# Kernel optimization log

Hardware: AMD Instinct MI355X
Metric: run time of the kernel (lower is better)

## Reference

```python
import jax, jax.numpy as jnp
import numpy as np
import math

B, S, DIM = 4, 1024, 4096
N_HEADS, N_KV_HEADS = 32, 8
HEAD_DIM = DIM // N_HEADS  # 128
PAST = 1024
N_REP = N_HEADS // N_KV_HEADS


def _rope_freqs(seq_len, head_dim, theta=10000.0):
    inv = 1.0 / (theta ** (np.arange(0, head_dim, 2, dtype=np.float32) / head_dim))
    t = np.arange(seq_len, dtype=np.float32)
    ang = np.outer(t, inv)  # (S, head_dim//2)
    return jnp.asarray(np.cos(ang)), jnp.asarray(np.sin(ang))


def setup_inputs() -> dict:
    key = jax.random.key(0)
    ks = jax.random.split(key, 8)
    sc = 0.02
    x = jax.random.normal(ks[0], (B, S, DIM), dtype=jnp.float32)
    freqs_cos, freqs_sin = _rope_freqs(S, HEAD_DIM)
    cache_k = jax.random.normal(ks[1], (B, N_KV_HEADS, PAST, HEAD_DIM), dtype=jnp.float32)
    cache_v = jax.random.normal(ks[2], (B, N_KV_HEADS, PAST, HEAD_DIM), dtype=jnp.float32)
    wq = jax.random.normal(ks[3], (DIM, DIM), dtype=jnp.float32) * sc
    wk = jax.random.normal(ks[4], (N_KV_HEADS * HEAD_DIM, DIM), dtype=jnp.float32) * sc
    wv = jax.random.normal(ks[5], (N_KV_HEADS * HEAD_DIM, DIM), dtype=jnp.float32) * sc
    wo = jax.random.normal(ks[6], (DIM, DIM), dtype=jnp.float32) * sc
    return {"x": x, "freqs_cos": freqs_cos, "freqs_sin": freqs_sin,
            "cache_k": cache_k, "cache_v": cache_v,
            "wq": wq, "wk": wk, "wv": wv, "wo": wo}


def _apply_rotary(x, cos, sin):
    # x: (b, h, s, d); cos/sin: (s, d//2) broadcast to (1, 1, s, d//2)
    xr = x.reshape(*x.shape[:-1], -1, 2)
    x_r, x_i = xr[..., 0], xr[..., 1]
    cos = cos[None, None, :, :]
    sin = sin[None, None, :, :]
    out_r = x_r * cos - x_i * sin
    out_i = x_r * sin + x_i * cos
    return jnp.stack([out_r, out_i], axis=-1).reshape(x.shape)


def reference(x, freqs_cos, freqs_sin, cache_k, cache_v, wq, wk, wv, wo):
    bsz, seqlen, _ = x.shape
    xq = x @ wq.T  # (b, s, n_heads*hd)
    xk = x @ wk.T  # (b, s, n_kv*hd)
    xv = x @ wv.T
    xq = xq.reshape(bsz, seqlen, N_HEADS, HEAD_DIM).transpose(0, 2, 1, 3)
    xk = xk.reshape(bsz, seqlen, N_KV_HEADS, HEAD_DIM).transpose(0, 2, 1, 3)
    xv = xv.reshape(bsz, seqlen, N_KV_HEADS, HEAD_DIM).transpose(0, 2, 1, 3)
    xq = _apply_rotary(xq, freqs_cos, freqs_sin)
    xk = _apply_rotary(xk, freqs_cos, freqs_sin)
    keys = jnp.concatenate([cache_k, xk], axis=2)    # (b, kvh, past+s, hd)
    values = jnp.concatenate([cache_v, xv], axis=2)
    keys = jnp.repeat(keys, N_REP, axis=1)            # (b, h, kv, hd)
    values = jnp.repeat(values, N_REP, axis=1)
    scores = jnp.einsum('bhsd,bhkd->bhsk', xq, keys) / math.sqrt(HEAD_DIM)
    scores = jax.nn.softmax(scores, axis=-1)          # no mask (inference path)
    out = jnp.einsum('bhsk,bhkd->bhsd', scores, values)
    out = out.transpose(0, 2, 1, 3).reshape(bsz, seqlen, -1)
    return out @ wo.T
```

## Files before the change

### kernel.cpp

```cpp
#include <hip/hip_runtime.h>
#include <hip/hip_bf16.h>

using bf16 = __hip_bfloat16;
typedef __attribute__((ext_vector_type(4))) float f4;
typedef __attribute__((ext_vector_type(16))) float f16v;
typedef __attribute__((ext_vector_type(8))) short s8v;
typedef __attribute__((ext_vector_type(4))) short s4v;
typedef __attribute__((ext_vector_type(4))) unsigned int u4v;
typedef unsigned int u32;

__device__ __forceinline__ short f2bf(float x) {
  bf16 h = __float2bfloat16(x);
  return *reinterpret_cast<short*>(&h);
}

__device__ __forceinline__ u32 pkbf(float lo, float hi) {
  return (u32)(unsigned short)f2bf(lo) | ((u32)(unsigned short)f2bf(hi) << 16);
}

__device__ __forceinline__ void gload16(const bf16* g, bf16* l) {
  __builtin_amdgcn_global_load_lds(
      (const __attribute__((address_space(1))) u32*)g,
      (__attribute__((address_space(3))) u32*)l, 16, 0, 0);
}

__device__ __forceinline__ void swp32(u32& a, u32& b, int h) {
#if __has_builtin(__builtin_amdgcn_permlane32_swap)
  typedef __attribute__((ext_vector_type(2))) int i2v;
  i2v r = __builtin_amdgcn_permlane32_swap((int)a, (int)b, false, false);
  a = (u32)r.x;
  b = (u32)r.y;
#else
  u32 as = (u32)__shfl_xor((int)a, 32), bs = (u32)__shfl_xor((int)b, 32);
  u32 an = h ? bs : a, bn = h ? b : as;
  a = an;
  b = bn;
#endif
}

__device__ __forceinline__ float xhalf_max(float x) {
#if __has_builtin(__builtin_amdgcn_permlane32_swap)
  typedef __attribute__((ext_vector_type(2))) int i2v;
  i2v r = __builtin_amdgcn_permlane32_swap(__float_as_int(x), __float_as_int(x),
                                           false, false);
  return fmaxf(__int_as_float(r.x), __int_as_float(r.y));
#else
  return fmaxf(x, __shfl_xor(x, 32));
#endif
}
__device__ __forceinline__ float xhalf_sum(float x) {
#if __has_builtin(__builtin_amdgcn_permlane32_swap)
  typedef __attribute__((ext_vector_type(2))) int i2v;
  i2v r = __builtin_amdgcn_permlane32_swap(__float_as_int(x), __float_as_int(x),
                                           false, false);
  return __int_as_float(r.x) + __int_as_float(r.y);
#else
  return x + __shfl_xor(x, 32);
#endif
}

__global__ __launch_bounds__(256) void cvt_bf16(const float* __restrict__ src,
                                                bf16* __restrict__ dst) {
  size_t e = ((size_t)blockIdx.x * 256 + threadIdx.x) << 3;
  f4 a = *(const f4*)(src + e);
  f4 b = *(const f4*)(src + e + 4);
  s8v r = { f2bf(a[0]), f2bf(a[1]), f2bf(a[2]), f2bf(a[3]),
            f2bf(b[0]), f2bf(b[1]), f2bf(b[2]), f2bf(b[3]) };
  *(s8v*)(dst + e) = r;
}

__global__ __launch_bounds__(256) void cvt_cache_k(const float* __restrict__ src,
                                                   bf16* __restrict__ dst) {
  size_t e = ((size_t)blockIdx.x * 256 + threadIdx.x) << 2;
  f4 v = *(const f4*)(src + e);
  unsigned d = (unsigned)(e & 127u), p = (unsigned)((e >> 7) & 1023u), bk = (unsigned)(e >> 17);
  s4v r = { f2bf(v[0]), f2bf(v[1]), f2bf(v[2]), f2bf(v[3]) };
  *(s4v*)(dst + (((size_t)bk * 2048 + p) << 7) + d) = r;
}

__global__ __launch_bounds__(256) void cvt_cache_v(const float* __restrict__ src,
                                                   bf16* __restrict__ dst) {
  size_t e = ((size_t)blockIdx.x * 256 + threadIdx.x) << 2;
  unsigned p = (unsigned)(e & 1023u), d = (unsigned)((e >> 10) & 127u), bk = (unsigned)(e >> 17);
  const float* s = src + (((size_t)bk * 1024 + p) << 7) + d;
  s4v r = { f2bf(s[0]), f2bf(s[128]), f2bf(s[256]), f2bf(s[384]) };
  *(s4v*)(dst + (((size_t)bk * 128 + d) << 11) + p) = r;
}

__global__ __launch_bounds__(256) void rope_kernel(bf16* __restrict__ buf,
                                                   const float* __restrict__ fc,
                                                   const float* __restrict__ fs,
                                                   int sstride, int soff) {
  size_t t = (size_t)blockIdx.x * 256 + threadIdx.x;
  unsigned ip = (unsigned)(t & 63u);
  unsigned s  = (unsigned)((t >> 6) & 1023u);
  unsigned hh = (unsigned)(t >> 16);
  size_t base = ((size_t)hh * sstride + soff + s) * 128 + 2 * ip;
  unsigned u = *(unsigned*)(buf + base);
  float xr = __uint_as_float(u << 16);
  float xi = __uint_as_float(u & 0xffff0000u);
  float c = fc[s * 64 + ip], sn = fs[s * 64 + ip];
  unsigned short r0 = (unsigned short)f2bf(xr * c - xi * sn);
  unsigned short r1 = (unsigned short)f2bf(xr * sn + xi * c);
  *(unsigned*)(buf + base) = (unsigned)r0 | ((unsigned)r1 << 16);
}

#define MODE_QKV 0
#define MODE_OUT 1

#define PHASE_TAIL(AC, BC, KS, MH)                                           \
  {                                                                          \
    s8v af[4], bv[4];                                                        \
    const int cofs = ((((KS) * 4) | g) ^ fx) << 3;                           \
    _Pragma("unroll") for (int mi = 0; mi < 4; ++mi)                         \
        af[mi] = *(const s8v*)&(AC)[aRowBase + ((MH)*4 + mi) * 1024 + cofs]; \
    _Pragma("unroll") for (int ni = 0; ni < 4; ++ni)                         \
        bv[ni] = *(const s8v*)&(BC)[bRowBase + ni * 1024 + cofs];            \
    __builtin_amdgcn_s_barrier();                                            \
    asm volatile("s_waitcnt lgkmcnt(0)" ::: "memory");                       \
    __builtin_amdgcn_s_setprio(1);                                           \
    _Pragma("unroll") for (int mi = 0; mi < 4; ++mi)                         \
      _Pragma("unroll") for (int ni = 0; ni < 4; ++ni)                       \
          acc[(MH)*4 + mi][ni] = __builtin_amdgcn_mfma_f32_16x16x32_bf16(    \
              af[mi], bv[ni], acc[(MH)*4 + mi][ni], 0, 0, 0);                \
    __builtin_amdgcn_s_setprio(0);                                           \
    __builtin_amdgcn_s_barrier();                                            \
  }

#define PHASE_HEAD(AC, BC)                                                   \
  {                                                                          \
    __builtin_amdgcn_s_barrier();                                            \
    s8v af[4], bv[4];                                                        \
    const int cofs = (g ^ fx) << 3;                                          \
    _Pragma("unroll") for (int mi = 0; mi < 4; ++mi)                         \
        af[mi] = *(const s8v*)&(AC)[aRowBase + mi * 1024 + cofs];            \
    _Pragma("unroll") for (int ni = 0; ni < 4; ++ni)                         \
        bv[ni] = *(const s8v*)&(BC)[bRowBase + ni * 1024 + cofs];            \
    asm volatile("s_waitcnt lgkmcnt(0)" ::: "memory");                       \
    __builtin_amdgcn_s_setprio(1);                                           \
    _Pragma("unroll") for (int mi = 0; mi < 4; ++mi)                         \
      _Pragma("unroll") for (int ni = 0; ni < 4; ++ni)                       \
          acc[mi][ni] = __builtin_amdgcn_mfma_f32_16x16x32_bf16(             \
              af[mi], bv[ni], acc[mi][ni], 0, 0, 0);                         \
    __builtin_amdgcn_s_setprio(0);                                           \
    __builtin_amdgcn_s_barrier();                                            \
  }

#define KTILE(AC, BC, PA, PB, NA, NB, PF)                                    \
  {                                                                          \
    if (PF) { gload16((NA), (PA)); gload16((NA) + rstep, (PA) + 4096); }     \
    if (PF) asm volatile("s_waitcnt vmcnt(2)" ::: "memory");                 \
    else    asm volatile("s_waitcnt vmcnt(0)" ::: "memory");                 \
    PHASE_HEAD(AC, BC)                                                       \
    if (PF) { gload16((NA) + 2 * rstep, (PA) + 8192);                        \
              gload16((NA) + 3 * rstep, (PA) + 12288); }                     \
    PHASE_TAIL(AC, BC, 0, 1)                                                 \
    if (PF) { gload16((NB), (PB)); gload16((NB) + rstep, (PB) + 4096); }     \
    PHASE_TAIL(AC, BC, 1, 0)                                                 \
    if (PF) { gload16((NB) + 2 * rstep, (PB) + 8192);                        \
              gload16((NB) + 3 * rstep, (PB) + 12288); }                     \
    PHASE_TAIL(AC, BC, 1, 1)                                                 \
  }

template <int MODE>
__global__ __launch_bounds__(512, 2) void gemm256(const bf16* __restrict__ A,
                                                  const bf16* __restrict__ B,
                                                  void* __restrict__ o1,
                                                  void* __restrict__ o2,
                                                  void* __restrict__ o3,
                                                  int K, float scale) {
  extern __shared__ bf16 smem[];
  bf16* A0 = smem;
  bf16* A1 = smem + 16384;
  bf16* B0 = smem + 32768;
  bf16* B1 = smem + 49152;

  const int tid = threadIdx.x;
  const int lane = tid & 63;
  const int wid = tid >> 6;
  const int wm = wid >> 2, wn = wid & 3;
  const int fr = lane & 15;
  const int g = lane >> 4;
  const int rg = g << 2;
  const int fx = lane & 7;

  const int gy = gridDim.y;
  int lin = blockIdx.y * gridDim.x + blockIdx.x;
  const int qq = (gridDim.x * gy) >> 3;
  lin = (lin & 7) * qq + (lin >> 3);
  const int bm = lin / gy;
  const int bn = lin % gy;

  const int r0 = tid >> 3;
  const int sc = (tid & 7) ^ (r0 & 7);
  const bf16* aptr = A + (size_t)(bm * 256 + r0) * K + sc * 8;
  const bf16* bptr = B + (size_t)(bn * 256 + r0) * K + sc * 8;
  const size_t rstep = (size_t)64 * K;
  const int wofs = (tid & 448) << 3;
  bf16* pA0 = A0 + wofs; bf16* pA1 = A1 + wofs;
  bf16* pB0 = B0 + wofs; bf16* pB1 = B1 + wofs;

  const int aRowBase = (wm * 128 + fr) * 64;
  const int bRowBase = (wn * 64 + fr) * 64;

  f4 acc[8][4] = {};

#pragma unroll
  for (int i = 0; i < 4; ++i) gload16(aptr + i * rstep, pA0 + i * 4096);
#pragma unroll
  for (int i = 0; i < 4; ++i) gload16(bptr + i * rstep, pB0 + i * 4096);

  const int nk = K >> 6;
  for (int kt = 0; kt < nk; kt += 2) {
    const bf16* na = aptr + (kt + 1) * 64;
    const bf16* nb = bptr + (kt + 1) * 64;
    KTILE(A0, B0, pA1, pB1, na, nb, true)
    const bool pf2 = (kt + 2 < nk);
    const bf16* na2 = aptr + (kt + 2) * 64;
    const bf16* nb2 = bptr + (kt + 2) * 64;
    KTILE(A1, B1, pA0, pB0, na2, nb2, pf2)
  }

#pragma unroll
  for (int m = 0; m < 8; ++m) {
    const int grow0 = bm * 256 + wm * 128 + m * 16 + rg;
    const int b = grow0 >> 10, s0 = grow0 & 1023;
#pragma unroll
    for (int n = 0; n < 4; ++n) {
      const int gcol = bn * 256 + wn * 64 + n * 16 + fr;
      if constexpr (MODE == MODE_OUT) {
#pragma unroll
        for (int j = 0; j < 4; ++j)
          ((float*)o1)[(size_t)(grow0 + j) * 4096 + gcol] = acc[m][n][j];
      } else {
        if (gcol < 4096) {
          const int h = gcol >> 7, d = gcol & 127;
#pragma unroll
          for (int j = 0; j < 4; ++j)
            ((bf16*)o1)[((((size_t)b * 32 + h) << 10) + s0 + j) * 128 + d] =
                __float2bfloat16(acc[m][n][j] * scale);
        } else if (gcol < 5120) {
          const int c = gcol - 4096, hv = c >> 7, d = c & 127;
#pragma unroll
          for (int j = 0; j < 4; ++j)
            ((bf16*)o2)[(((size_t)b * 8 + hv) * 2048 + 1024 + s0 + j) * 128 + d] =
                __float2bfloat16(acc[m][n][j]);
        } else {
          const int c = gcol - 5120, hv = c >> 7, d = c & 127;
          s4v r = { f2bf(acc[m][n][0]), f2bf(acc[m][n][1]),
                    f2bf(acc[m][n][2]), f2bf(acc[m][n][3]) };
          *(s4v*)((bf16*)o3 + (((size_t)b * 8 + hv) * 128 + d) * 2048 + 1024 + s0) = r;
        }
      }
    }
  }
}

__global__ __launch_bounds__(512) void attn_kernel(const bf16* __restrict__ Q,
                                                   const bf16* __restrict__ Kf,
                                                   const bf16* __restrict__ Vt,
                                                   bf16* __restrict__ O) {
  __shared__ alignas(16) bf16 Kls[2][8192];
  __shared__ alignas(16) bf16 Vls[2][8192];

  const int tid = threadIdx.x;
  const int lane = tid & 63;
  const int w = tid >> 6;
  const int h = lane >> 5;
  const int q31 = lane & 31;
  const int rx = q31 & 7;

  const int qb = blockIdx.x;
  const int bh = blockIdx.y;
  const int b = bh >> 5, hd = bh & 31;
  const int kv = hd >> 2;

  const size_t qbase = (((size_t)b * 32 + hd) << 10) * 128;
  const size_t kbase = (((size_t)b * 8 + kv) * 2048) * 128;
  const size_t vbase = (((size_t)b * 8 + kv) * 128) * 2048;

  const int qrow = qb * 256 + w * 32 + q31;
  s8v qf[8];
#pragma unroll
  for (int c = 0; c < 8; ++c)
    qf[c] = *(const s8v*)&Q[qbase + (size_t)qrow * 128 + c * 16 + h * 8];

  const int sr = tid >> 3;
  const int swz8 = (((tid & 7) ^ (sr & 7)) << 3);
  const int wbase = w * 512;

  f16v oacc[4] = {};
  float mrun = -3e38f, lrun = 0.f;

  auto stage = [&](int kb, int bufi) {
    const bf16* ksrc = Kf + kbase + (size_t)(kb * 64 + sr) * 128 + swz8;
    gload16(ksrc,      &Kls[bufi][wbase]);
    gload16(ksrc + 64, &Kls[bufi][4096 + wbase]);
    const bf16* vsrc = Vt + vbase + (size_t)sr * 2048 + kb * 64 + swz8;
    gload16(vsrc,                      &Vls[bufi][wbase]);
    gload16(vsrc + (size_t)64 * 2048,  &Vls[bufi][4096 + wbase]);
  };

  stage(0, 0);
  asm volatile("s_waitcnt vmcnt(0)" ::: "memory");
  __syncthreads();

  for (int kb = 0; kb < 32; ++kb) {
    const int bufi = kb & 1;
    if (kb + 1 < 32) stage(kb + 1, bufi ^ 1);

    const bf16* KB = Kls[bufi];
    const bf16* VB = Vls[bufi];

    f16v sac[2] = {};
    __builtin_amdgcn_s_setprio(1);
#pragma unroll
    for (int c = 0; c < 8; ++c) {
      const int cc = 2 * c + h;
      const int cof = (cc >> 3) * 4096 + (((cc & 7) ^ rx) << 3);
      s8v k0 = *(const s8v*)&KB[cof + q31 * 64];
      s8v k1 = *(const s8v*)&KB[cof + (32 + q31) * 64];
      sac[0] = __builtin_amdgcn_mfma_f32_32x32x16_bf16(k0, qf[c], sac[0], 0, 0, 0);
      sac[1] = __builtin_amdgcn_mfma_f32_32x32x16_bf16(k1, qf[c], sac[1], 0, 0, 0);
    }
    __builtin_amdgcn_s_setprio(0);

    float pm = -3e38f;
#pragma unroll
    for (int r = 0; r < 16; ++r) {
      pm = fmaxf(pm, sac[0][r]);
      pm = fmaxf(pm, sac[1][r]);
    }
    pm = xhalf_max(pm);

    const bool skip = __all(pm <= mrun + 8.0f);
    if (!skip) {
      const float mnew = fmaxf(mrun, pm);
      const float corr = exp2f(mrun - mnew);
      mrun = mnew;
      lrun *= corr;
#pragma unroll
      for (int m = 0; m < 4; ++m)
#pragma unroll
        for (int r = 0; r < 16; ++r) oacc[m][r] *= corr;
    }
    float ls = 0.f;
#pragma unroll
    for (int s = 0; s < 2; ++s)
#pragma unroll
      for (int r = 0; r < 16; ++r) {
        const float p = exp2f(sac[s][r] - mrun);
        sac[s][r] = p;
        ls += p;
      }
    lrun += xhalf_sum(ls);

    s8v F[4];
#pragma unroll
    for (int s = 0; s < 2; ++s) {
      u32 W[8];
#pragma unroll
      for (int t = 0; t < 8; ++t) W[t] = pkbf(sac[s][2 * t], sac[s][2 * t + 1]);
      swp32(W[0], W[2], h); swp32(W[1], W[3], h);
      swp32(W[4], W[6], h); swp32(W[5], W[7], h);
      union { u32 u[4]; s8v v; } f0, f1;
      f0.u[0] = W[0]; f0.u[1] = W[1]; f0.u[2] = W[2]; f0.u[3] = W[3];
      f1.u[0] = W[4]; f1.u[1] = W[5]; f1.u[2] = W[6]; f1.u[3] = W[7];
      F[s * 2] = f0.v;
      F[s * 2 + 1] = f1.v;
    }

    __builtin_amdgcn_s_setprio(1);
#pragma unroll
    for (int ksg = 0; ksg < 4; ++ksg) {
      const int cc2 = 2 * ksg + h;
      const int vof = ((cc2 ^ rx) << 3);
#pragma unroll
      for (int m = 0; m < 4; ++m) {
        s8v vf = *(const s8v*)&VB[(m * 32 + q31) * 64 + vof];
        oacc[m] = __builtin_amdgcn_mfma_f32_32x32x16_bf16(vf, F[ksg], oacc[m], 0, 0, 0);
      }
    }
    __builtin_amdgcn_s_setprio(0);

    asm volatile("s_waitcnt vmcnt(0)" ::: "memory");
    __syncthreads();
  }

  const float inv = 1.f / lrun;
  bf16* orow = O + ((size_t)b * 1024 + qrow) * 4096 + hd * 128;
#pragma unroll
  for (int m = 0; m < 4; ++m)
#pragma unroll
    for (int r = 0; r < 16; r += 2) {
      const int d = m * 32 + (r & 3) + 8 * (r >> 2) + 4 * h;
      *(u32*)&orow[d] = pkbf(oacc[m][r] * inv, oacc[m][r + 1] * inv);
    }
}

extern "C" void kernel_launch(void* const* d_in, const int* in_sizes, int n_in,
                              void* d_out, int out_size, void* d_ws, size_t ws_size,
                              hipStream_t stream) {
  const float* x  = (const float*)d_in[0];
  const float* fc = (const float*)d_in[1];
  const float* fs = (const float*)d_in[2];
  const float* ck = (const float*)d_in[3];
  const float* cv = (const float*)d_in[4];
  const float* wq = (const float*)d_in[5];
  const float* wk = (const float*)d_in[6];
  const float* wv = (const float*)d_in[7];
  const float* wo = (const float*)d_in[8];
  float* out = (float*)d_out;

  char* ws = (char*)d_ws;
  bf16* qr    = (bf16*)(ws);
  bf16* kfull = (bf16*)(ws + (32u << 20));
  bf16* vt    = (bf16*)(ws + (48u << 20));
  bf16* xb    = (bf16*)(ws + (64u << 20));
  bf16* attn  = xb;
  bf16* wqb   = (bf16*)(ws + (96u << 20));
  bf16* wob   = wqb;
  bf16* wkvb  = (bf16*)(ws + (128u << 20));

  hipFuncSetAttribute(reinterpret_cast<const void*>(&gemm256<MODE_QKV>),
                      hipFuncAttributeMaxDynamicSharedMemorySize, 131072);
  hipFuncSetAttribute(reinterpret_cast<const void*>(&gemm256<MODE_OUT>),
                      hipFuncAttributeMaxDynamicSharedMemorySize, 131072);

  cvt_bf16<<<8192, 256, 0, stream>>>(x, xb);
  cvt_bf16<<<8192, 256, 0, stream>>>(wq, wqb);
  cvt_bf16<<<2048, 256, 0, stream>>>(wk, wkvb);
  cvt_bf16<<<2048, 256, 0, stream>>>(wv, wkvb + 4194304);
  cvt_cache_k<<<4096, 256, 0, stream>>>(ck, kfull);
  cvt_cache_v<<<4096, 256, 0, stream>>>(cv, vt);

  gemm256<MODE_QKV><<<dim3(16, 24), 512, 131072, stream>>>(
      xb, wqb, qr, kfull, vt, 4096, 0.1275174198520337f);

  cvt_bf16<<<8192, 256, 0, stream>>>(wo, wob);

  rope_kernel<<<32768, 256, 0, stream>>>(qr, fc, fs, 1024, 0);
  rope_kernel<<<8192, 256, 0, stream>>>(kfull, fc, fs, 2048, 1024);

  attn_kernel<<<dim3(4, 128), 512, 0, stream>>>(qr, kfull, vt, attn);

  gemm256<MODE_OUT><<<dim3(16, 16), 512, 131072, stream>>>(
      attn, wob, out, nullptr, nullptr, 4096, 1.0f);
}
```

Measured before the change: 667.5 us.

## Split fused QKV GEMM into Q GEMM and 128x256-tile KV GEMM; remap attention blocks

The fused QKV projection launched a 16x24 grid of 256x256 tiles. With 128KB of LDS per block, that is about one and a half waves across the CUs, so the last wave runs partly empty. The projection is now two launches: a 16x16 Q GEMM, and a new KV GEMM with 128x256 tiles and 96KB of LDS that writes K and transposed V directly. The attention grid is also remapped so the four query heads sharing a KV head run close together, to improve cache reuse of K and V. The cost is an extra kernel launch and a second, less-tuned GEMM variant.

New measurement: 619.9 us. 1.08x faster.

```diff
diff --git a/kernel.cpp b/kernel.cpp
--- a/kernel.cpp
+++ b/kernel.cpp
@@ -105,7 +105,7 @@
   *(unsigned*)(buf + base) = (unsigned)r0 | ((unsigned)r1 << 16);
 }
 
-#define MODE_QKV 0
+#define MODE_Q   0
 #define MODE_OUT 1
 
 #define PHASE_TAIL(AC, BC, KS, MH)                                           \
@@ -166,8 +166,6 @@
 __global__ __launch_bounds__(512, 2) void gemm256(const bf16* __restrict__ A,
                                                   const bf16* __restrict__ B,
                                                   void* __restrict__ o1,
-                                                  void* __restrict__ o2,
-                                                  void* __restrict__ o3,
                                                   int K, float scale) {
   extern __shared__ bf16 smem[];
   bf16* A0 = smem;
@@ -233,24 +231,122 @@
         for (int j = 0; j < 4; ++j)
           ((float*)o1)[(size_t)(grow0 + j) * 4096 + gcol] = acc[m][n][j];
       } else {
-        if (gcol < 4096) {
-          const int h = gcol >> 7, d = gcol & 127;
-#pragma unroll
-          for (int j = 0; j < 4; ++j)
-            ((bf16*)o1)[((((size_t)b * 32 + h) << 10) + s0 + j) * 128 + d] =
-                __float2bfloat16(acc[m][n][j] * scale);
-        } else if (gcol < 5120) {
-          const int c = gcol - 4096, hv = c >> 7, d = c & 127;
-#pragma unroll
-          for (int j = 0; j < 4; ++j)
-            ((bf16*)o2)[(((size_t)b * 8 + hv) * 2048 + 1024 + s0 + j) * 128 + d] =
-                __float2bfloat16(acc[m][n][j]);
-        } else {
-          const int c = gcol - 5120, hv = c >> 7, d = c & 127;
-          s4v r = { f2bf(acc[m][n][0]), f2bf(acc[m][n][1]),
-                    f2bf(acc[m][n][2]), f2bf(acc[m][n][3]) };
-          *(s4v*)((bf16*)o3 + (((size_t)b * 8 + hv) * 128 + d) * 2048 + 1024 + s0) = r;
-        }
+        const int h = gcol >> 7, d = gcol & 127;
+#pragma unroll
+        for (int j = 0; j < 4; ++j)
+          ((bf16*)o1)[((((size_t)b * 32 + h) << 10) + s0 + j) * 128 + d] =
+              __float2bfloat16(acc[m][n][j] * scale);
+      }
+    }
+  }
+}
+
+#define PH128(AC, BC, KS, OPEN)                                              \
+  {                                                                          \
+    if (OPEN) __builtin_amdgcn_s_barrier();                                  \
+    s8v af[4], bv[4];                                                        \
+    const int cofs = ((((KS) * 4) | g) ^ fx) << 3;                           \
+    _Pragma("unroll") for (int mi = 0; mi < 4; ++mi)                         \
+        af[mi] = *(const s8v*)&(AC)[aRowBase + mi * 1024 + cofs];            \
+    _Pragma("unroll") for (int ni = 0; ni < 4; ++ni)                         \
+        bv[ni] = *(const s8v*)&(BC)[bRowBase + ni * 1024 + cofs];            \
+    if (!(OPEN)) __builtin_amdgcn_s_barrier();                               \
+    asm volatile("s_waitcnt lgkmcnt(0)" ::: "memory");                       \
+    __builtin_amdgcn_s_setprio(1);                                           \
+    _Pragma("unroll") for (int mi = 0; mi < 4; ++mi)                         \
+      _Pragma("unroll") for (int ni = 0; ni < 4; ++ni)                       \
+          acc[mi][ni] = __builtin_amdgcn_mfma_f32_16x16x32_bf16(             \
+              af[mi], bv[ni], acc[mi][ni], 0, 0, 0);                         \
+    __builtin_amdgcn_s_setprio(0);                                           \
+    __builtin_amdgcn_s_barrier();                                            \
+  }
+
+#define KTILE128(AC, BC, PA, PB, NA, NB, PF)                                 \
+  {                                                                          \
+    if (PF) { gload16((NB), (PB)); gload16((NB) + rstep, (PB) + 4096); }     \
+    if (PF) asm volatile("s_waitcnt vmcnt(2)" ::: "memory");                 \
+    else    asm volatile("s_waitcnt vmcnt(0)" ::: "memory");                 \
+    PH128(AC, BC, 0, true)                                                   \
+    if (PF) { gload16((NB) + 2 * rstep, (PB) + 8192);                        \
+              gload16((NB) + 3 * rstep, (PB) + 12288);                       \
+              gload16((NA), (PA)); gload16((NA) + rstep, (PA) + 4096); }     \
+    PH128(AC, BC, 1, false)                                                  \
+  }
+
+__global__ __launch_bounds__(512, 2) void gemm128kv(const bf16* __restrict__ A,
+                                                    const bf16* __restrict__ B,
+                                                    bf16* __restrict__ kout,
+                                                    bf16* __restrict__ vout,
+                                                    int K) {
+  extern __shared__ bf16 smem[];
+  bf16* A0 = smem;
+  bf16* A1 = smem + 8192;
+  bf16* B0 = smem + 16384;
+  bf16* B1 = smem + 32768;
+
+  const int tid = threadIdx.x;
+  const int lane = tid & 63;
+  const int wid = tid >> 6;
+  const int wm = wid >> 2, wn = wid & 3;
+  const int fr = lane & 15;
+  const int g = lane >> 4;
+  const int rg = g << 2;
+  const int fx = lane & 7;
+
+  const int gy = gridDim.y;
+  int lin = blockIdx.y * gridDim.x + blockIdx.x;
+  const int qq = (gridDim.x * gy) >> 3;
+  lin = (lin & 7) * qq + (lin >> 3);
+  const int bm = lin / gy;
+  const int bn = lin % gy;
+
+  const int r0 = tid >> 3;
+  const int sc = (tid & 7) ^ (r0 & 7);
+  const bf16* aptr = A + (size_t)(bm * 128 + r0) * K + sc * 8;
+  const bf16* bptr = B + (size_t)(bn * 256 + r0) * K + sc * 8;
+  const size_t rstep = (size_t)64 * K;
+  const int wofs = (tid & 448) << 3;
+  bf16* pA0 = A0 + wofs; bf16* pA1 = A1 + wofs;
+  bf16* pB0 = B0 + wofs; bf16* pB1 = B1 + wofs;
+
+  const int aRowBase = (wm * 64 + fr) * 64;
+  const int bRowBase = (wn * 64 + fr) * 64;
+
+  f4 acc[4][4] = {};
+
+  gload16(aptr, pA0); gload16(aptr + rstep, pA0 + 4096);
+#pragma unroll
+  for (int i = 0; i < 4; ++i) gload16(bptr + i * rstep, pB0 + i * 4096);
+
+  const int nk = K >> 6;
+  for (int kt = 0; kt < nk; kt += 2) {
+    const bf16* na = aptr + (kt + 1) * 64;
+    const bf16* nb = bptr + (kt + 1) * 64;
+    KTILE128(A0, B0, pA1, pB1, na, nb, true)
+    const bool pf2 = (kt + 2 < nk);
+    const bf16* na2 = aptr + (kt + 2) * 64;
+    const bf16* nb2 = bptr + (kt + 2) * 64;
+    KTILE128(A1, B1, pA0, pB0, na2, nb2, pf2)
+  }
+
+#pragma unroll
+  for (int m = 0; m < 4; ++m) {
+    const int grow0 = bm * 128 + wm * 64 + m * 16 + rg;
+    const int b = grow0 >> 10, s0 = grow0 & 1023;
+#pragma unroll
+    for (int n = 0; n < 4; ++n) {
+      const int gcol = bn * 256 + wn * 64 + n * 16 + fr;
+      if (gcol < 1024) {
+        const int hv = gcol >> 7, d = gcol & 127;
+#pragma unroll
+        for (int j = 0; j < 4; ++j)
+          kout[(((size_t)b * 8 + hv) * 2048 + 1024 + s0 + j) * 128 + d] =
+              __float2bfloat16(acc[m][n][j]);
+      } else {
+        const int c = gcol - 1024, hv = c >> 7, d = c & 127;
+        s4v r = { f2bf(acc[m][n][0]), f2bf(acc[m][n][1]),
+                  f2bf(acc[m][n][2]), f2bf(acc[m][n][3]) };
+        *(s4v*)(vout + (((size_t)b * 8 + hv) * 128 + d) * 2048 + 1024 + s0) = r;
       }
     }
   }
@@ -270,10 +366,13 @@
   const int q31 = lane & 31;
   const int rx = q31 & 7;
 
-  const int qb = blockIdx.x;
-  const int bh = blockIdx.y;
-  const int b = bh >> 5, hd = bh & 31;
-  const int kv = hd >> 2;
+  int lin = blockIdx.y * 4 + blockIdx.x;
+  lin = (lin & 7) * 64 + (lin >> 3);
+  const int qb = lin & 3;
+  const int hrem = (lin >> 2) & 3;
+  const int pair = lin >> 4;
+  const int b = pair >> 3, kv = pair & 7;
+  const int hd = kv * 4 + hrem;
 
   const size_t qbase = (((size_t)b * 32 + hd) << 10) * 128;
   const size_t kbase = (((size_t)b * 8 + kv) * 2048) * 128;
@@ -422,10 +521,12 @@
   bf16* wob   = wqb;
   bf16* wkvb  = (bf16*)(ws + (128u << 20));
 
-  hipFuncSetAttribute(reinterpret_cast<const void*>(&gemm256<MODE_QKV>),
+  hipFuncSetAttribute(reinterpret_cast<const void*>(&gemm256<MODE_Q>),
                       hipFuncAttributeMaxDynamicSharedMemorySize, 131072);
   hipFuncSetAttribute(reinterpret_cast<const void*>(&gemm256<MODE_OUT>),
                       hipFuncAttributeMaxDynamicSharedMemorySize, 131072);
+  hipFuncSetAttribute(reinterpret_cast<const void*>(&gemm128kv),
+                      hipFuncAttributeMaxDynamicSharedMemorySize, 98304);
 
   cvt_bf16<<<8192, 256, 0, stream>>>(x, xb);
   cvt_bf16<<<8192, 256, 0, stream>>>(wq, wqb);
@@ -434,8 +535,9 @@
   cvt_cache_k<<<4096, 256, 0, stream>>>(ck, kfull);
   cvt_cache_v<<<4096, 256, 0, stream>>>(cv, vt);
 
-  gemm256<MODE_QKV><<<dim3(16, 24), 512, 131072, stream>>>(
-      xb, wqb, qr, kfull, vt, 4096, 0.1275174198520337f);
+  gemm256<MODE_Q><<<dim3(16, 16), 512, 131072, stream>>>(
+      xb, wqb, qr, 4096, 0.1275174198520337f);
+  gemm128kv<<<dim3(32, 8), 512, 98304, stream>>>(xb, wkvb, kfull, vt, 4096);
 
   cvt_bf16<<<8192, 256, 0, stream>>>(wo, wob);
 
@@ -445,5 +547,5 @@
   attn_kernel<<<dim3(4, 128), 512, 0, stream>>>(qr, kfull, vt, attn);
 
   gemm256<MODE_OUT><<<dim3(16, 16), 512, 131072, stream>>>(
-      attn, wob, out, nullptr, nullptr, 4096, 1.0f);
-}
+      attn, wob, out, 4096, 1.0f);
+}
```
